# Performance work log

Hardware: AMD Instinct MI355X
Metric: run time of the kernel (lower is better)

## Reference

```python
import jax, jax.numpy as jnp
import numpy as np


def setup_inputs() -> dict:
    key = jax.random.key(0)
    ks = jax.random.split(key, 6)
    B, C, H, W, Q = 16, 64, 64, 64, 8192
    HID = 256
    K = C * 9  # 576, unfolded channel count and srnet out_dim (co_mat=1)
    feat = jax.random.normal(ks[0], (B, C, H, W), jnp.float32)
    coord = jax.random.uniform(ks[1], (B, Q, 2), jnp.float32) * 2.0 - 1.0  # normalized [-1,1]
    cell = jnp.ones((B, Q, 2), jnp.float32) * (2.0 / 128.0)  # HR cell size for 128-px grid
    w1 = jax.random.normal(ks[2], (3, HID), jnp.float32) / np.sqrt(3.0)
    b1 = jnp.zeros((HID,), jnp.float32)
    w2 = jax.random.normal(ks[3], (HID, HID), jnp.float32) / np.sqrt(float(HID))
    b2 = jnp.zeros((HID,), jnp.float32)
    w3 = jax.random.normal(ks[4], (HID, K), jnp.float32) / np.sqrt(float(HID))
    b3 = jnp.zeros((K,), jnp.float32)
    return {"feat": feat, "coord": coord, "cell": cell,
            "w1": w1, "b1": b1, "w2": w2, "b2": b2, "w3": w3, "b3": b3}


def reference(feat, coord, cell, w1, b1, w2, b2, w3, b3):
    B, C, H, W = feat.shape
    Q = coord.shape[1]
    K = C * 9
    co_mat = 1
    # F.unfold(feat, 3, padding=1).view(B, C*9, H, W): channel-major, kernel pos minor
    padded = jnp.pad(feat, ((0, 0), (0, 0), (1, 1), (1, 1)))
    patches = jnp.stack([padded[:, :, i:i + H, j:j + W]
                         for i in range(3) for j in range(3)], axis=2)  # [B,C,9,H,W]
    featu = patches.reshape(B, K, H * W)
    # shift query coords by half a cell
    coord_ = coord - cell / 2.0
    coord_q = jnp.clip(coord_ + 1e-6, -1.0 + 1e-6, 1.0 - 1e-6)
    # nearest grid_sample, align_corners=False: idx = round(((c+1)*S - 1)/2)
    # coord[...,0] indexes H (grid y after flip), coord[...,1] indexes W (grid x)
    iy = jnp.clip(jnp.round(((coord_q[..., 0] + 1.0) * H - 1.0) / 2.0), 0, H - 1).astype(jnp.int32)
    ix = jnp.clip(jnp.round(((coord_q[..., 1] + 1.0) * W - 1.0) / 2.0), 0, W - 1).astype(jnp.int32)
    lin = iy * W + ix  # [B,Q]
    q_feat = jnp.take_along_axis(featu, lin[:, None, :], axis=2).transpose(0, 2, 1)  # [B,Q,K]
    # q_coord: make_coord value minus half-pixel shift at the nearest index = 2i/S - 1 (exact)
    qy = 2.0 * iy.astype(jnp.float32) / H - 1.0
    qx = 2.0 * ix.astype(jnp.float32) / W - 1.0
    rel_y = (coord_[..., 0] - qy) * (H / 2.0)
    rel_x = (coord_[..., 1] - qx) * (W / 2.0)
    r_rev = cell[..., 0] * (H / 2.0)
    inp = jnp.stack([rel_y, rel_x, r_rev], axis=-1)  # [B,Q,3]
    # srnet MLP: per-query filter of shape [K, co_mat]
    h = jax.nn.relu(inp @ w1 + b1)
    h = jax.nn.relu(h @ w2 + b2)
    wmat = (h @ w3 + b3).reshape(B, Q, K, co_mat)
    # bmm combine: [1,K] @ [K,co_mat] per query
    pred = jnp.einsum('bqk,bqkc->bqc', q_feat, wmat)  # [B,Q,1]
    return pred
```

## Files before the change

### kernel.cpp

```cpp
#include <hip/hip_runtime.h>
#include <hip/hip_bf16.h>

#define BB 16
#define CC 64
#define HH 64
#define WW 64
#define QQ 8192
#define HID 256
#define KK 576
#define HT 66
#define FROW 264

typedef short short8 __attribute__((ext_vector_type(8)));
typedef short sv4    __attribute__((ext_vector_type(4)));
typedef float f32x4  __attribute__((ext_vector_type(4)));

__device__ __forceinline__ short f2bf(float f) {
    union { float f; unsigned u; } v; v.f = f;
    unsigned r = v.u + 0x7fffu + ((v.u >> 16) & 1u);
    return (short)(r >> 16);
}
__device__ __forceinline__ float bf2f(short s) {
    union { unsigned u; float f; } v; v.u = ((unsigned)(unsigned short)s) << 16;
    return v.f;
}
__device__ __forceinline__ void barrier_lds() {
    asm volatile("s_waitcnt lgkmcnt(0)" ::: "memory");
    __builtin_amdgcn_s_barrier();
    asm volatile("" ::: "memory");
}
__device__ __forceinline__ void glld16(const short* g, short* l) {
    __builtin_amdgcn_global_load_lds(
        (const __attribute__((address_space(1))) void*)g,
        (__attribute__((address_space(3))) void*)l, 16, 0, 0);
}

__global__ __launch_bounds__(256) void prep_transpose_k(const float* __restrict__ feat,
                                                        const float* __restrict__ w2,
                                                        const float* __restrict__ w3,
                                                        const float* __restrict__ b3,
                                                        short* __restrict__ featT,
                                                        short* __restrict__ w3cB,
                                                        short* __restrict__ w2cB) {
    __shared__ float ftile[64][65];
    const int t = threadIdx.x;
    const int gidx = blockIdx.x * 256 + t;

    if (gidx < 156672) {
        int kchunk = gidx / 2176;
        int rem = gidx - kchunk * 2176;
        int n = rem >> 3, j = rem & 7;
        int kglob = kchunk * 8 + j;
        int pos = kglob >> 6, c = kglob & 63;
        float v = 0.f;
        if (n < 256)      v = w3[n * KK + c * 9 + pos];
        else if (n == 256) v = b3[c * 9 + pos];
        w3cB[gidx] = f2bf(v);
    }
    if (gidx < 65536) {
        int kchunk = gidx >> 11;
        int rem = gidx & 2047;
        int n = rem >> 3, j = rem & 7;
        int k = kchunk * 8 + j;
        w2cB[gidx] = f2bf(w2[k * 256 + n]);
    }

    const int b = blockIdx.x / HT;
    const int yy = blockIdx.x - b * HT;
    short* out_row = featT + ((b * HT + yy) * HT) * 64;

    if (yy == 0 || yy == HT - 1) {
        for (int idx = t; idx < HT * 64; idx += 256) out_row[idx] = 0;
        return;
    }
    const int y = yy - 1;
    const float* src = feat + ((b * CC) * HH + y) * WW;
#pragma unroll
    for (int i = 0; i < 16; ++i) {
        int idx = i * 256 + t;
        int c = idx >> 6, x = idx & 63;
        ftile[c][x] = src[c * (HH * WW) + x];
    }
    if (t < 64) out_row[t] = 0;
    else if (t < 128) out_row[(HT - 1) * 64 + (t - 64)] = 0;
    __syncthreads();
#pragma unroll
    for (int i = 0; i < 16; ++i) {
        int idx = i * 256 + t;
        int x = idx >> 6, c = idx & 63;
        out_row[(x + 1) * 64 + c] = f2bf(ftile[c][x]);
    }
}

#define SSTR 72
__global__ __launch_bounds__(256, 2) void conv_k(const short* __restrict__ featT,
                                                 const short* __restrict__ w3cB,
                                                 short* __restrict__ F) {
    __shared__ short slab[3 * HT * SSTR];
    __shared__ short Bb[2][8704];
    const int t = threadIdx.x;
    const int wave = t >> 6, lane = t & 63, quad = lane >> 4, ln16 = lane & 15;
    const int b = blockIdx.x >> 6, y = blockIdx.x & 63;

    f32x4 acc[4][5];
#pragma unroll
    for (int a = 0; a < 4; ++a)
#pragma unroll
        for (int i = 0; i < 5; ++i) acc[a][i] = (f32x4){0.f, 0.f, 0.f, 0.f};

    auto stageB = [&](int buf, int st) {
        const short* src = w3cB + st * 8704;
#pragma unroll
        for (int u = 0; u < 5; ++u) {
            int cidx = (u < 4) ? (u * 4 + wave) : 16;
            if (u < 4 || wave == 0)
                glld16(src + cidx * 512 + lane * 8, &Bb[buf][cidx * 512]);
        }
    };

    stageB(0, 0);

    const short* slabsrc = featT + b * (HT * HT * 64) + y * (HT * 64);
#pragma unroll
    for (int it = 0; it < 7; ++it) {
        int i = it * 256 + t;
        if (i < 1584) {
            short8 v = *(const short8*)(slabsrc + i * 8);
            int row = i >> 3, cs = (i & 7) * 8;
            *(short8*)(&slab[row * SSTR + cs]) = v;
        }
    }
    __syncthreads();

#pragma unroll
    for (int st = 0; st < 18; ++st) {
        const int cur = st & 1;
        if (st < 17) stageB(cur ^ 1, st + 1);
        const int pos = st >> 1, ks = st & 1;
        const int di = pos / 3, dj = pos - di * 3;
        short8 af[4];
#pragma unroll
        for (int ms = 0; ms < 4; ++ms)
            af[ms] = *(const short8*)(&slab[(di * HT + ms * 16 + ln16 + dj) * SSTR + ks * 32 + quad * 8]);
#pragma unroll
        for (int i = 0; i < 5; ++i) {
            int sub = (i < 4) ? (wave + 4 * i) : 16;
            short8 bf = *(const short8*)(&Bb[cur][(quad * 272 + sub * 16 + ln16) * 8]);
#pragma unroll
            for (int ms = 0; ms < 4; ++ms)
                acc[ms][i] = __builtin_amdgcn_mfma_f32_16x16x32_bf16(af[ms], bf, acc[ms][i], 0, 0, 0);
        }
        __syncthreads();
    }

#pragma unroll
    for (int h = 0; h < 2; ++h) {
#pragma unroll
        for (int i = 0; i < 5; ++i) {
            int sub = (i < 4) ? (wave + 4 * i) : 16;
            int n = sub * 16 + ln16;
            bool store = (i < 4) || (wave == 0 && n < FROW);
            if (store) {
#pragma unroll
                for (int ms2 = 0; ms2 < 2; ++ms2) {
                    int ms = h * 2 + ms2;
#pragma unroll
                    for (int r = 0; r < 4; ++r) {
                        int xl = ms2 * 16 + quad * 4 + r;
                        slab[xl * FROW + n] = f2bf(acc[ms][i][r]);
                    }
                }
            }
        }
        __syncthreads();
        short8* dst = (short8*)(F + ((long)(b * 64 + y) * 64 + h * 32) * FROW);
        const short8* src8 = (const short8*)slab;
#pragma unroll
        for (int it = 0; it < 5; ++it) {
            int idx = it * 256 + t;
            if (idx < (32 * FROW) / 8) dst[idx] = src8[idx];
        }
        __syncthreads();
    }
}

#define HSPLIT 136
__global__ __launch_bounds__(256, 2) void mlp_k(const float* __restrict__ coord,
                                                const float* __restrict__ cell,
                                                const float* __restrict__ w1,
                                                const float* __restrict__ b1,
                                                const float* __restrict__ b2v,
                                                const short* __restrict__ w2cB,
                                                const short* __restrict__ F,
                                                float* __restrict__ out) {
    __shared__ short Hh[64 * HSPLIT];
    __shared__ short Wb[2][8192];
    __shared__ float red_s[64][4];

    const int t = threadIdx.x;
    const int wave = t >> 6, lane = t & 63, quad = lane >> 4, ln16 = lane & 15;
    const int qbase = blockIdx.x * 64;
    const int b = qbase >> 13;

    auto stageW = [&](int buf, int s) {
        const short* src = w2cB + s * 8192;
#pragma unroll
        for (int u = 0; u < 4; ++u) {
            int cidx = u * 4 + wave;
            glld16(src + cidx * 512 + lane * 8, &Wb[buf][cidx * 512]);
        }
    };

    stageW(0, 0);

    const int g = qbase + lane;
    const float2 cc = *(const float2*)(coord + g * 2);
    const float2 ce = *(const float2*)(cell + g * 2);
    const float coy = cc.x - ce.x * 0.5f, cox = cc.y - ce.y * 0.5f;
    const float cqy = fminf(fmaxf(coy + 1e-6f, -0.999999f), 0.999999f);
    const float cqx = fminf(fmaxf(cox + 1e-6f, -0.999999f), 0.999999f);
    int iy = (int)rintf(((cqy + 1.0f) * 64.0f - 1.0f) * 0.5f); iy = min(max(iy, 0), 63);
    int ix = (int)rintf(((cqx + 1.0f) * 64.0f - 1.0f) * 0.5f); ix = min(max(ix, 0), 63);
    const int lin = iy * 64 + ix;
    const float in0 = (coy - ((float)iy * (1.0f / 32.0f) - 1.0f)) * 32.0f;
    const float in1 = (cox - ((float)ix * (1.0f / 32.0f) - 1.0f)) * 32.0f;
    const float in2 = ce.x * 32.0f;

    short8 hv[8];
    const int k0w = wave * 64;
#pragma unroll
    for (int c8 = 0; c8 < 8; ++c8) {
        const int k0 = k0w + c8 * 8;
        f32x4 wa0 = *(const f32x4*)(w1 + k0),       wa1 = *(const f32x4*)(w1 + k0 + 4);
        f32x4 wb0 = *(const f32x4*)(w1 + 256 + k0), wb1 = *(const f32x4*)(w1 + 256 + k0 + 4);
        f32x4 wc0 = *(const f32x4*)(w1 + 512 + k0), wc1 = *(const f32x4*)(w1 + 512 + k0 + 4);
        f32x4 bb0 = *(const f32x4*)(b1 + k0),       bb1 = *(const f32x4*)(b1 + k0 + 4);
#pragma unroll
        for (int jj = 0; jj < 4; ++jj) {
            float v0 = fmaf(in0, wa0[jj], fmaf(in1, wb0[jj], fmaf(in2, wc0[jj], bb0[jj])));
            float v1 = fmaf(in0, wa1[jj], fmaf(in1, wb1[jj], fmaf(in2, wc1[jj], bb1[jj])));
            hv[c8][jj]     = f2bf(fmaxf(v0, 0.f));
            hv[c8][jj + 4] = f2bf(fmaxf(v1, 0.f));
        }
    }
    if (wave < 2) {
#pragma unroll
        for (int c8 = 0; c8 < 8; ++c8)
            *(short8*)(&Hh[lane * HSPLIT + wave * 64 + c8 * 8]) = hv[c8];
    }
    f32x4 b2q[4];
#pragma unroll
    for (int i = 0; i < 4; ++i)
        b2q[i] = *(const f32x4*)(b2v + wave * 64 + i * 16 + quad * 4);
    __syncthreads();

    f32x4 acc2[4][4];
#pragma unroll
    for (int i = 0; i < 4; ++i)
#pragma unroll
        for (int ms = 0; ms < 4; ++ms) acc2[i][ms] = (f32x4){0.f, 0.f, 0.f, 0.f};
#pragma unroll
    for (int s = 0; s < 8; ++s) {
        const int cur = s & 1;
        if (s < 7) stageW(cur ^ 1, s + 1);
        short8 wf[4], hf[4];
#pragma unroll
        for (int i = 0; i < 4; ++i)
            wf[i] = *(const short8*)(&Wb[cur][(quad * 256 + wave * 64 + i * 16 + ln16) * 8]);
        const int col = (s & 3) * 32 + quad * 8;
#pragma unroll
        for (int ms = 0; ms < 4; ++ms)
            hf[ms] = *(const short8*)(&Hh[(ms * 16 + ln16) * HSPLIT + col]);
#pragma unroll
        for (int i = 0; i < 4; ++i)
#pragma unroll
            for (int ms = 0; ms < 4; ++ms)
                acc2[i][ms] = __builtin_amdgcn_mfma_f32_16x16x32_bf16(wf[i], hf[ms], acc2[i][ms], 0, 0, 0);
        if (s == 3) {
            __syncthreads();
            if (wave >= 2) {
#pragma unroll
                for (int c8 = 0; c8 < 8; ++c8)
                    *(short8*)(&Hh[lane * HSPLIT + (wave - 2) * 64 + c8 * 8]) = hv[c8];
            }
            barrier_lds();
        } else if (s < 7) {
            __syncthreads();
        }
    }

    const short* Fb = F + (long)b * 4096 * FROW;
    sv4 fv[4][4];
#pragma unroll
    for (int ms = 0; ms < 4; ++ms) {
        int linm = __shfl(lin, ms * 16 + ln16, 64);
        const short* Fr = Fb + (long)linm * FROW + wave * 64 + quad * 4;
#pragma unroll
        for (int i = 0; i < 4; ++i) fv[ms][i] = *(const sv4*)(Fr + i * 16);
    }
    const float fbv = bf2f(Fb[(long)lin * FROW + 256]);

    float part[4] = {0.f, 0.f, 0.f, 0.f};
#pragma unroll
    for (int i = 0; i < 4; ++i)
#pragma unroll
        for (int ms = 0; ms < 4; ++ms)
#pragma unroll
            for (int r = 0; r < 4; ++r)
                part[ms] = fmaf(fmaxf(acc2[i][ms][r] + b2q[i][r], 0.f), bf2f(fv[ms][i][r]), part[ms]);
#pragma unroll
    for (int ms = 0; ms < 4; ++ms) {
        part[ms] += __shfl_xor(part[ms], 16, 64);
        part[ms] += __shfl_xor(part[ms], 32, 64);
    }
    if (quad == 0) {
#pragma unroll
        for (int ms = 0; ms < 4; ++ms) red_s[ms * 16 + ln16][wave] = part[ms];
    }
    barrier_lds();
    if (t < 64)
        out[qbase + t] = red_s[t][0] + red_s[t][1] + red_s[t][2] + red_s[t][3] + fbv;
}

extern "C" void kernel_launch(void* const* d_in, const int* in_sizes, int n_in,
                              void* d_out, int out_size, void* d_ws, size_t ws_size,
                              hipStream_t stream) {
    const float* feat  = (const float*)d_in[0];
    const float* coord = (const float*)d_in[1];
    const float* cell  = (const float*)d_in[2];
    const float* w1    = (const float*)d_in[3];
    const float* b1    = (const float*)d_in[4];
    const float* w2    = (const float*)d_in[5];
    const float* b2    = (const float*)d_in[6];
    const float* w3    = (const float*)d_in[7];
    const float* b3    = (const float*)d_in[8];
    float* out = (float*)d_out;

    char* ws = (char*)d_ws;
    short* w3cB  = (short*)(ws);
    short* w2cB  = (short*)(ws + 313344);
    short* featT = (short*)(ws + 444416);
    short* F     = (short*)(ws + 9365504);
    (void)ws_size; (void)in_sizes; (void)n_in; (void)out_size;

    prep_transpose_k<<<BB * HT, 256, 0, stream>>>(feat, w2, w3, b3, featT, w3cB, w2cB);
    conv_k<<<BB * HH, 256, 0, stream>>>(featT, w3cB, F);
    mlp_k<<<(BB * QQ) / 64, 256, 0, stream>>>(coord, cell, w1, b1, b2, w2cB, F, out);
}
```

Measured before the change: 157.7 us.

## Double block tiles in conv and MLP kernels to share staged weights

Both conv_k and mlp_k now run 512 threads per block. Each block covers two output rows or 128 queries, with the second group of four waves taking the second M tile. The staged w3/w2 weight slabs in LDS are now shared by twice as many rows, which halves the global weight traffic and the staging work per output. The cost is more LDS per block, a larger slab and Hh buffer, and fewer blocks. The launch bound asks for 4 blocks per CU at 512 threads, which tightens the register budget and could cause spills.

```diff
diff --git a/kernel.cpp b/kernel.cpp
--- a/kernel.cpp
+++ b/kernel.cpp
@@ -93,14 +93,16 @@
 }
 
 #define SSTR 72
-__global__ __launch_bounds__(256, 2) void conv_k(const short* __restrict__ featT,
+__global__ __launch_bounds__(512, 4) void conv_k(const short* __restrict__ featT,
                                                  const short* __restrict__ w3cB,
                                                  short* __restrict__ F) {
-    __shared__ short slab[3 * HT * SSTR];
+    __shared__ short slab[4 * HT * SSTR];
     __shared__ short Bb[2][8704];
     const int t = threadIdx.x;
     const int wave = t >> 6, lane = t & 63, quad = lane >> 4, ln16 = lane & 15;
-    const int b = blockIdx.x >> 6, y = blockIdx.x & 63;
+    const int mh = wave >> 2, nq = wave & 3;
+    const int b = blockIdx.x >> 5;
+    const int y0 = (blockIdx.x & 31) * 2;
 
     f32x4 acc[4][5];
 #pragma unroll
@@ -111,23 +113,23 @@
     auto stageB = [&](int buf, int st) {
         const short* src = w3cB + st * 8704;
 #pragma unroll
-        for (int u = 0; u < 5; ++u) {
-            int cidx = (u < 4) ? (u * 4 + wave) : 16;
-            if (u < 4 || wave == 0)
-                glld16(src + cidx * 512 + lane * 8, &Bb[buf][cidx * 512]);
-        }
+        for (int u = 0; u < 2; ++u) {
+            int cidx = u * 8 + wave;
+            glld16(src + cidx * 512 + lane * 8, &Bb[buf][cidx * 512]);
+        }
+        if (wave == 0)
+            glld16(src + 16 * 512 + lane * 8, &Bb[buf][16 * 512]);
     };
 
     stageB(0, 0);
 
-    const short* slabsrc = featT + b * (HT * HT * 64) + y * (HT * 64);
-#pragma unroll
-    for (int it = 0; it < 7; ++it) {
-        int i = it * 256 + t;
-        if (i < 1584) {
+    const short* slabsrc = featT + b * (HT * HT * 64) + y0 * (HT * 64);
+#pragma unroll
+    for (int it = 0; it < 5; ++it) {
+        int i = it * 512 + t;
+        if (i < 2112) {
             short8 v = *(const short8*)(slabsrc + i * 8);
-            int row = i >> 3, cs = (i & 7) * 8;
-            *(short8*)(&slab[row * SSTR + cs]) = v;
+            *(short8*)(&slab[(i >> 3) * SSTR + (i & 7) * 8]) = v;
         }
     }
     __syncthreads();
@@ -141,10 +143,10 @@
         short8 af[4];
 #pragma unroll
         for (int ms = 0; ms < 4; ++ms)
-            af[ms] = *(const short8*)(&slab[(di * HT + ms * 16 + ln16 + dj) * SSTR + ks * 32 + quad * 8]);
+            af[ms] = *(const short8*)(&slab[((mh + di) * HT + ms * 16 + ln16 + dj) * SSTR + ks * 32 + quad * 8]);
 #pragma unroll
         for (int i = 0; i < 5; ++i) {
-            int sub = (i < 4) ? (wave + 4 * i) : 16;
+            int sub = (i < 4) ? (nq + 4 * i) : 16;
             short8 bf = *(const short8*)(&Bb[cur][(quad * 272 + sub * 16 + ln16) * 8]);
 #pragma unroll
             for (int ms = 0; ms < 4; ++ms)
@@ -155,37 +157,37 @@
 
 #pragma unroll
     for (int h = 0; h < 2; ++h) {
-#pragma unroll
-        for (int i = 0; i < 5; ++i) {
-            int sub = (i < 4) ? (wave + 4 * i) : 16;
-            int n = sub * 16 + ln16;
-            bool store = (i < 4) || (wave == 0 && n < FROW);
-            if (store) {
-#pragma unroll
-                for (int ms2 = 0; ms2 < 2; ++ms2) {
-                    int ms = h * 2 + ms2;
-#pragma unroll
-                    for (int r = 0; r < 4; ++r) {
-                        int xl = ms2 * 16 + quad * 4 + r;
-                        slab[xl * FROW + n] = f2bf(acc[ms][i][r]);
-                    }
+        if (mh == h) {
+#pragma unroll
+            for (int i = 0; i < 5; ++i) {
+                int sub = (i < 4) ? (nq + 4 * i) : 16;
+                int n = sub * 16 + ln16;
+                bool store = (i < 4) || (nq == 0 && n < FROW);
+                if (store) {
+#pragma unroll
+                    for (int ms = 0; ms < 4; ++ms)
+#pragma unroll
+                        for (int r = 0; r < 4; ++r) {
+                            int xl = ms * 16 + quad * 4 + r;
+                            slab[xl * FROW + n] = f2bf(acc[ms][i][r]);
+                        }
                 }
             }
         }
         __syncthreads();
-        short8* dst = (short8*)(F + ((long)(b * 64 + y) * 64 + h * 32) * FROW);
+        short8* dst = (short8*)(F + (long)((b * 64 + y0 + h) * 64) * FROW);
         const short8* src8 = (const short8*)slab;
 #pragma unroll
         for (int it = 0; it < 5; ++it) {
-            int idx = it * 256 + t;
-            if (idx < (32 * FROW) / 8) dst[idx] = src8[idx];
+            int idx = it * 512 + t;
+            if (idx < (64 * FROW) / 8) dst[idx] = src8[idx];
         }
         __syncthreads();
     }
 }
 
 #define HSPLIT 136
-__global__ __launch_bounds__(256, 2) void mlp_k(const float* __restrict__ coord,
+__global__ __launch_bounds__(512, 4) void mlp_k(const float* __restrict__ coord,
                                                 const float* __restrict__ cell,
                                                 const float* __restrict__ w1,
                                                 const float* __restrict__ b1,
@@ -193,27 +195,29 @@
                                                 const short* __restrict__ w2cB,
                                                 const short* __restrict__ F,
                                                 float* __restrict__ out) {
-    __shared__ short Hh[64 * HSPLIT];
+    __shared__ short Hh[128 * HSPLIT];
     __shared__ short Wb[2][8192];
-    __shared__ float red_s[64][4];
+    __shared__ float red_s[128][4];
+    __shared__ float fbv_s[128];
 
     const int t = threadIdx.x;
     const int wave = t >> 6, lane = t & 63, quad = lane >> 4, ln16 = lane & 15;
-    const int qbase = blockIdx.x * 64;
-    const int b = qbase >> 13;
+    const int mh = wave >> 2, nq = wave & 3;
+    const int qbase = blockIdx.x * 128;
+    const int b = blockIdx.x >> 6;
 
     auto stageW = [&](int buf, int s) {
         const short* src = w2cB + s * 8192;
 #pragma unroll
-        for (int u = 0; u < 4; ++u) {
-            int cidx = u * 4 + wave;
+        for (int u = 0; u < 2; ++u) {
+            int cidx = u * 8 + wave;
             glld16(src + cidx * 512 + lane * 8, &Wb[buf][cidx * 512]);
         }
     };
 
     stageW(0, 0);
 
-    const int g = qbase + lane;
+    const int g = qbase + mh * 64 + lane;
     const float2 cc = *(const float2*)(coord + g * 2);
     const float2 ce = *(const float2*)(cell + g * 2);
     const float coy = cc.x - ce.x * 0.5f, cox = cc.y - ce.y * 0.5f;
@@ -227,7 +231,7 @@
     const float in2 = ce.x * 32.0f;
 
     short8 hv[8];
-    const int k0w = wave * 64;
+    const int k0w = nq * 64;
 #pragma unroll
     for (int c8 = 0; c8 < 8; ++c8) {
         const int k0 = k0w + c8 * 8;
@@ -243,15 +247,15 @@
             hv[c8][jj + 4] = f2bf(fmaxf(v1, 0.f));
         }
     }
-    if (wave < 2) {
+    if (nq < 2) {
 #pragma unroll
         for (int c8 = 0; c8 < 8; ++c8)
-            *(short8*)(&Hh[lane * HSPLIT + wave * 64 + c8 * 8]) = hv[c8];
+            *(short8*)(&Hh[(mh * 64 + lane) * HSPLIT + nq * 64 + c8 * 8]) = hv[c8];
     }
     f32x4 b2q[4];
 #pragma unroll
     for (int i = 0; i < 4; ++i)
-        b2q[i] = *(const f32x4*)(b2v + wave * 64 + i * 16 + quad * 4);
+        b2q[i] = *(const f32x4*)(b2v + nq * 64 + i * 16 + quad * 4);
     __syncthreads();
 
     f32x4 acc2[4][4];
@@ -266,11 +270,11 @@
         short8 wf[4], hf[4];
 #pragma unroll
         for (int i = 0; i < 4; ++i)
-            wf[i] = *(const short8*)(&Wb[cur][(quad * 256 + wave * 64 + i * 16 + ln16) * 8]);
+            wf[i] = *(const short8*)(&Wb[cur][(quad * 256 + nq * 64 + i * 16 + ln16) * 8]);
         const int col = (s & 3) * 32 + quad * 8;
 #pragma unroll
         for (int ms = 0; ms < 4; ++ms)
-            hf[ms] = *(const short8*)(&Hh[(ms * 16 + ln16) * HSPLIT + col]);
+            hf[ms] = *(const short8*)(&Hh[(mh * 64 + ms * 16 + ln16) * HSPLIT + col]);
 #pragma unroll
         for (int i = 0; i < 4; ++i)
 #pragma unroll
@@ -278,10 +282,10 @@
                 acc2[i][ms] = __builtin_amdgcn_mfma_f32_16x16x32_bf16(wf[i], hf[ms], acc2[i][ms], 0, 0, 0);
         if (s == 3) {
             __syncthreads();
-            if (wave >= 2) {
+            if (nq >= 2) {
 #pragma unroll
                 for (int c8 = 0; c8 < 8; ++c8)
-                    *(short8*)(&Hh[lane * HSPLIT + (wave - 2) * 64 + c8 * 8]) = hv[c8];
+                    *(short8*)(&Hh[(mh * 64 + lane) * HSPLIT + (nq - 2) * 64 + c8 * 8]) = hv[c8];
             }
             barrier_lds();
         } else if (s < 7) {
@@ -294,11 +298,10 @@
 #pragma unroll
     for (int ms = 0; ms < 4; ++ms) {
         int linm = __shfl(lin, ms * 16 + ln16, 64);
-        const short* Fr = Fb + (long)linm * FROW + wave * 64 + quad * 4;
+        const short* Fr = Fb + (long)linm * FROW + nq * 64 + quad * 4;
 #pragma unroll
         for (int i = 0; i < 4; ++i) fv[ms][i] = *(const sv4*)(Fr + i * 16);
     }
-    const float fbv = bf2f(Fb[(long)lin * FROW + 256]);
 
     float part[4] = {0.f, 0.f, 0.f, 0.f};
 #pragma unroll
@@ -315,11 +318,13 @@
     }
     if (quad == 0) {
 #pragma unroll
-        for (int ms = 0; ms < 4; ++ms) red_s[ms * 16 + ln16][wave] = part[ms];
-    }
+        for (int ms = 0; ms < 4; ++ms) red_s[mh * 64 + ms * 16 + ln16][nq] = part[ms];
+    }
+    if (nq == 0)
+        fbv_s[mh * 64 + lane] = bf2f(Fb[(long)lin * FROW + 256]);
     barrier_lds();
-    if (t < 64)
-        out[qbase + t] = red_s[t][0] + red_s[t][1] + red_s[t][2] + red_s[t][3] + fbv;
+    if (t < 128)
+        out[qbase + t] = red_s[t][0] + red_s[t][1] + red_s[t][2] + red_s[t][3] + fbv_s[t];
 }
 
 extern "C" void kernel_launch(void* const* d_in, const int* in_sizes, int n_in,
@@ -344,6 +349,6 @@
     (void)ws_size; (void)in_sizes; (void)n_in; (void)out_size;
 
     prep_transpose_k<<<BB * HT, 256, 0, stream>>>(feat, w2, w3, b3, featT, w3cB, w2cB);
-    conv_k<<<BB * HH, 256, 0, stream>>>(featT, w3cB, F);
-    mlp_k<<<(BB * QQ) / 64, 256, 0, stream>>>(coord, cell, w1, b1, b2, w2cB, F, out);
-}
+    conv_k<<<BB * 32, 512, 0, stream>>>(featT, w3cB, F);
+    mlp_k<<<(BB * QQ) / 128, 512, 0, stream>>>(coord, cell, w1, b1, b2, w2cB, F, out);
+}
```

New measurement: 184.1 us. +16.8%, slower.

## Halve conv LDS slab via channel-split staging; raise occupancy of conv and MLP kernels

Applied to the files above, without the earlier changes.

The weight prep reorders the K dimension so the first nine k-steps use channels 0-31 and the last nine use channels 32-63. The conv kernel can then hold only a 32-channel slab in LDS and restage the second half mid-loop. The conv and B buffers now share one LDS array, and both kernels move to launch_bounds(256,3) to fit more blocks per CU. The MLP kernel stops keeping layer-1 activations in registers across the GEMM and recomputes them in the upper waves, freeing registers. The cost is an extra barrier and slab reload in conv and duplicated layer-1 math in MLP.

```diff
diff --git a/kernel.cpp b/kernel.cpp
--- a/kernel.cpp
+++ b/kernel.cpp
@@ -51,7 +51,10 @@
         int rem = gidx - kchunk * 2176;
         int n = rem >> 3, j = rem & 7;
         int kglob = kchunk * 8 + j;
-        int pos = kglob >> 6, c = kglob & 63;
+        int khalf = kglob / 288;
+        int r2 = kglob - khalf * 288;
+        int pos = r2 >> 5;
+        int c = khalf * 32 + (r2 & 31);
         float v = 0.f;
         if (n < 256)      v = w3[n * KK + c * 9 + pos];
         else if (n == 256) v = b3[c * 9 + pos];
@@ -92,12 +95,12 @@
     }
 }
 
-#define SSTR 72
-__global__ __launch_bounds__(256, 2) void conv_k(const short* __restrict__ featT,
+#define SST2 36
+__global__ __launch_bounds__(256, 3) void conv_k(const short* __restrict__ featT,
                                                  const short* __restrict__ w3cB,
                                                  short* __restrict__ F) {
-    __shared__ short slab[3 * HT * SSTR];
-    __shared__ short Bb[2][8704];
+    __shared__ short SH[24536];
+    short* slab = SH;
     const int t = threadIdx.x;
     const int wave = t >> 6, lane = t & 63, quad = lane >> 4, ln16 = lane & 15;
     const int b = blockIdx.x >> 6, y = blockIdx.x & 63;
@@ -110,47 +113,57 @@
 
     auto stageB = [&](int buf, int st) {
         const short* src = w3cB + st * 8704;
+        short* dstb = SH + 7128 + buf * 8704;
 #pragma unroll
         for (int u = 0; u < 5; ++u) {
             int cidx = (u < 4) ? (u * 4 + wave) : 16;
             if (u < 4 || wave == 0)
-                glld16(src + cidx * 512 + lane * 8, &Bb[buf][cidx * 512]);
+                glld16(src + cidx * 512 + lane * 8, dstb + cidx * 512);
         }
     };
+    const short* slabsrc = featT + b * (HT * HT * 64) + y * (HT * 64);
+    auto stageA = [&](int kh) {
+#pragma unroll
+        for (int it = 0; it < 4; ++it) {
+            int i = it * 256 + t;
+            if (i < 792) {
+                int r = i >> 2, s = (i & 3) * 8;
+                short8 v = *(const short8*)(slabsrc + r * 64 + kh * 32 + s);
+                *(short8*)(&slab[r * SST2 + s]) = v;
+            }
+        }
+    };
 
     stageB(0, 0);
-
-    const short* slabsrc = featT + b * (HT * HT * 64) + y * (HT * 64);
-#pragma unroll
-    for (int it = 0; it < 7; ++it) {
-        int i = it * 256 + t;
-        if (i < 1584) {
-            short8 v = *(const short8*)(slabsrc + i * 8);
-            int row = i >> 3, cs = (i & 7) * 8;
-            *(short8*)(&slab[row * SSTR + cs]) = v;
-        }
-    }
+    stageA(0);
     __syncthreads();
 
 #pragma unroll
     for (int st = 0; st < 18; ++st) {
         const int cur = st & 1;
         if (st < 17) stageB(cur ^ 1, st + 1);
-        const int pos = st >> 1, ks = st & 1;
+        const int pos = (st < 9) ? st : (st - 9);
         const int di = pos / 3, dj = pos - di * 3;
+        const short* Bc = SH + 7128 + cur * 8704;
         short8 af[4];
 #pragma unroll
         for (int ms = 0; ms < 4; ++ms)
-            af[ms] = *(const short8*)(&slab[(di * HT + ms * 16 + ln16 + dj) * SSTR + ks * 32 + quad * 8]);
+            af[ms] = *(const short8*)(&slab[(di * HT + ms * 16 + ln16 + dj) * SST2 + quad * 8]);
 #pragma unroll
         for (int i = 0; i < 5; ++i) {
             int sub = (i < 4) ? (wave + 4 * i) : 16;
-            short8 bf = *(const short8*)(&Bb[cur][(quad * 272 + sub * 16 + ln16) * 8]);
+            short8 bf = *(const short8*)(Bc + (quad * 272 + sub * 16 + ln16) * 8);
 #pragma unroll
             for (int ms = 0; ms < 4; ++ms)
                 acc[ms][i] = __builtin_amdgcn_mfma_f32_16x16x32_bf16(af[ms], bf, acc[ms][i], 0, 0, 0);
         }
-        __syncthreads();
+        if (st == 8) {
+            __syncthreads();
+            stageA(1);
+            barrier_lds();
+        } else {
+            __syncthreads();
+        }
     }
 
 #pragma unroll
@@ -167,14 +180,14 @@
 #pragma unroll
                     for (int r = 0; r < 4; ++r) {
                         int xl = ms2 * 16 + quad * 4 + r;
-                        slab[xl * FROW + n] = f2bf(acc[ms][i][r]);
+                        SH[xl * FROW + n] = f2bf(acc[ms][i][r]);
                     }
                 }
             }
         }
         __syncthreads();
         short8* dst = (short8*)(F + ((long)(b * 64 + y) * 64 + h * 32) * FROW);
-        const short8* src8 = (const short8*)slab;
+        const short8* src8 = (const short8*)SH;
 #pragma unroll
         for (int it = 0; it < 5; ++it) {
             int idx = it * 256 + t;
@@ -185,7 +198,7 @@
 }
 
 #define HSPLIT 136
-__global__ __launch_bounds__(256, 2) void mlp_k(const float* __restrict__ coord,
+__global__ __launch_bounds__(256, 3) void mlp_k(const float* __restrict__ coord,
                                                 const float* __restrict__ cell,
                                                 const float* __restrict__ w1,
                                                 const float* __restrict__ b1,
@@ -226,28 +239,29 @@
     const float in1 = (cox - ((float)ix * (1.0f / 32.0f) - 1.0f)) * 32.0f;
     const float in2 = ce.x * 32.0f;
 
-    short8 hv[8];
-    const int k0w = wave * 64;
-#pragma unroll
-    for (int c8 = 0; c8 < 8; ++c8) {
-        const int k0 = k0w + c8 * 8;
-        f32x4 wa0 = *(const f32x4*)(w1 + k0),       wa1 = *(const f32x4*)(w1 + k0 + 4);
-        f32x4 wb0 = *(const f32x4*)(w1 + 256 + k0), wb1 = *(const f32x4*)(w1 + 256 + k0 + 4);
-        f32x4 wc0 = *(const f32x4*)(w1 + 512 + k0), wc1 = *(const f32x4*)(w1 + 512 + k0 + 4);
-        f32x4 bb0 = *(const f32x4*)(b1 + k0),       bb1 = *(const f32x4*)(b1 + k0 + 4);
-#pragma unroll
-        for (int jj = 0; jj < 4; ++jj) {
-            float v0 = fmaf(in0, wa0[jj], fmaf(in1, wb0[jj], fmaf(in2, wc0[jj], bb0[jj])));
-            float v1 = fmaf(in0, wa1[jj], fmaf(in1, wb1[jj], fmaf(in2, wc1[jj], bb1[jj])));
-            hv[c8][jj]     = f2bf(fmaxf(v0, 0.f));
-            hv[c8][jj + 4] = f2bf(fmaxf(v1, 0.f));
-        }
-    }
-    if (wave < 2) {
-#pragma unroll
-        for (int c8 = 0; c8 < 8; ++c8)
-            *(short8*)(&Hh[lane * HSPLIT + wave * 64 + c8 * 8]) = hv[c8];
-    }
+    auto computeH1_write = [&]() {
+        const int kbase = wave * 64;
+        const int col = (wave & 1) * 64;
+#pragma unroll
+        for (int c8 = 0; c8 < 8; ++c8) {
+            const int k0 = kbase + c8 * 8;
+            f32x4 wa0 = *(const f32x4*)(w1 + k0),       wa1 = *(const f32x4*)(w1 + k0 + 4);
+            f32x4 wb0 = *(const f32x4*)(w1 + 256 + k0), wb1 = *(const f32x4*)(w1 + 256 + k0 + 4);
+            f32x4 wc0 = *(const f32x4*)(w1 + 512 + k0), wc1 = *(const f32x4*)(w1 + 512 + k0 + 4);
+            f32x4 bb0 = *(const f32x4*)(b1 + k0),       bb1 = *(const f32x4*)(b1 + k0 + 4);
+            short8 hv;
+#pragma unroll
+            for (int jj = 0; jj < 4; ++jj) {
+                float v0 = fmaf(in0, wa0[jj], fmaf(in1, wb0[jj], fmaf(in2, wc0[jj], bb0[jj])));
+                float v1 = fmaf(in0, wa1[jj], fmaf(in1, wb1[jj], fmaf(in2, wc1[jj], bb1[jj])));
+                hv[jj]     = f2bf(fmaxf(v0, 0.f));
+                hv[jj + 4] = f2bf(fmaxf(v1, 0.f));
+            }
+            *(short8*)(&Hh[lane * HSPLIT + col + c8 * 8]) = hv;
+        }
+    };
+
+    if (wave < 2) computeH1_write();
     f32x4 b2q[4];
 #pragma unroll
     for (int i = 0; i < 4; ++i)
@@ -278,11 +292,7 @@
                 acc2[i][ms] = __builtin_amdgcn_mfma_f32_16x16x32_bf16(wf[i], hf[ms], acc2[i][ms], 0, 0, 0);
         if (s == 3) {
             __syncthreads();
-            if (wave >= 2) {
-#pragma unroll
-                for (int c8 = 0; c8 < 8; ++c8)
-                    *(short8*)(&Hh[lane * HSPLIT + (wave - 2) * 64 + c8 * 8]) = hv[c8];
-            }
+            if (wave >= 2) computeH1_write();
             barrier_lds();
         } else if (s < 7) {
             __syncthreads();
```

Measured after the change: 174.9 us. 10.9% more time.
